# Kernel optimization log

Measured on AMD Instinct MI355X. Metric: run time of the kernel, lower is better.

The kernel has to match this reference:

```python
import jax, jax.numpy as jnp
import numpy as np

N_VARS = 2048
BATCH = 1024


def encode_input(pos):
    # pos: [n_vars, batch] -> [2*n_vars + 2, batch]
    # row 0 = 0, row 1 = 1, even rows >=2 = pos, odd rows >=3 = 1 - pos
    n = pos.shape[0]
    out = jnp.zeros((2 * n + 2,) + pos.shape[1:], dtype=pos.dtype)
    out = out.at[1].set(1.0)
    out = out.at[2::2].set(pos)
    out = out.at[3::2].set(1.0 - pos)
    return out


def setup_inputs() -> dict:
    key = jax.random.key(0)
    k0, k1, k2, k3, k4 = jax.random.split(key, 5)
    x = jax.random.uniform(k0, (N_VARS, BATCH), dtype=jnp.float32)
    idx0 = jax.random.randint(k1, (32768, 2), 0, 2 * N_VARS + 2, dtype=jnp.int32)
    idx1 = jax.random.randint(k2, (16384, 2), 0, 32768, dtype=jnp.int32)
    idx2 = jax.random.randint(k3, (8192, 2), 0, 16384, dtype=jnp.int32)
    idx3 = jax.random.randint(k4, (4096, 2), 0, 8192, dtype=jnp.int32)
    return {"x": x, "idx0": idx0, "idx1": idx1, "idx2": idx2, "idx3": idx3}


def reference(x, idx0, idx1, idx2, idx3):
    h = encode_input(x)                  # [2*n_vars+2, B]
    h = h[idx0].prod(axis=1)             # ProductLayer: [32768, B]
    h = h[idx1].sum(axis=1)              # SumLayer:     [16384, B]
    h = h[idx2].prod(axis=1)             # ProductLayer: [8192, B]
    h = h[idx3].sum(axis=1)              # SumLayer:     [4096, B]
    return h
```

## Files before the change

kernel.cpp:

```cpp
#include <hip/hip_runtime.h>
#include <hip/hip_fp16.h>

#define BATCH  1024
#define NVARS  2048
#define N_OUT  4096

typedef float f32x4 __attribute__((ext_vector_type(4)));

__device__ __forceinline__ __half2 u2h2(unsigned u) {
    union { unsigned u; __half2 h; } c; c.u = u; return c.h;
}
__device__ __forceinline__ unsigned h22u(__half2 h) {
    union { unsigned u; __half2 h; } c; c.h = h; return c.u;
}

__global__ void prep_kernel(const float* __restrict__ x,
                            const int2* __restrict__ idx0,
                            const int2* __restrict__ idx1,
                            const int2* __restrict__ idx2,
                            const int2* __restrict__ idx3,
                            unsigned* __restrict__ T,
                            unsigned* __restrict__ xh)
{
    const int gtid = blockIdx.x * blockDim.x + threadIdx.x;

    {
        const float4* x4 = (const float4*)x;
        float4 a = x4[(size_t)gtid * 2];
        float4 b = x4[(size_t)gtid * 2 + 1];
        uint4 w;
        w.x = h22u(__floats2half2_rn(a.x, a.y));
        w.y = h22u(__floats2half2_rn(a.z, a.w));
        w.z = h22u(__floats2half2_rn(b.x, b.y));
        w.w = h22u(__floats2half2_rn(b.z, b.w));
        reinterpret_cast<uint4*>(xh)[gtid] = w;
    }

    if (gtid < N_OUT) {
        const int i = gtid;
        int2 p3 = idx3[i];
        int n = 0;
        #pragma unroll
        for (int t = 0; t < 2; ++t) {
            int2 p2 = idx2[t ? p3.y : p3.x];
            #pragma unroll
            for (int u = 0; u < 2; ++u) {
                int2 p1 = idx1[u ? p2.y : p2.x];
                #pragma unroll
                for (int v = 0; v < 2; ++v) {
                    int2 p0 = idx0[v ? p1.y : p1.x];
                    unsigned w = 0;
                    #pragma unroll
                    for (int e = 0; e < 2; ++e) {
                        int k = e ? p0.y : p0.x;
                        unsigned code;
                        if (k < 2) code = (unsigned)k << 11;
                        else       code = ((2u + (k & 1)) << 11) | ((unsigned)(k - 2) >> 1);
                        w |= code << (16 * e);
                    }
                    T[(size_t)i * 8 + n] = w;
                    ++n;
                }
            }
        }
    }
}

__device__ __forceinline__ void sel2sc(unsigned sel, unsigned& s, unsigned& c) {
    c = (sel & 1u) ? 0x3C003C00u : 0u;
    s = (sel == 2u) ? 0x3C003C00u : (sel == 3u) ? 0xBC00BC00u : 0u;
}

__global__ __launch_bounds__(256) void knowledge_main(
    const char* __restrict__ xh,
    const uint4* __restrict__ T4,
    float* __restrict__ out)
{
    const int bx  = blockIdx.x;
    const int tid = threadIdx.x;
    const int octet = bx & 15;
    const int o     = (bx >> 4) * 32 + (tid >> 3);
    const int cg    = octet * 8 + (tid & 7);
    const char* base = xh + cg * 16;

    uint4 t0 = T4[(size_t)o * 2];
    uint4 t1 = T4[(size_t)o * 2 + 1];
    const unsigned tw[8] = {t0.x, t0.y, t0.z, t0.w, t1.x, t1.y, t1.z, t1.w};

    uint4 Aw[8], Bw[8];
    #pragma unroll
    for (int m = 0; m < 8; ++m) {
        unsigned w = tw[m];
        Aw[m] = *reinterpret_cast<const uint4*>(base + ((w & 0x7FFu) << 11));
        Bw[m] = *reinterpret_cast<const uint4*>(base + (((w >> 16) & 0x7FFu) << 11));
    }

    float2 accf[4];
    #pragma unroll
    for (int k = 0; k < 4; ++k) accf[k] = make_float2(0.f, 0.f);

    #pragma unroll
    for (int a3 = 0; a3 < 2; ++a3) {
        __half2 prod2[4];
        #pragma unroll
        for (int a2 = 0; a2 < 2; ++a2) {
            __half2 sum1[4];
            #pragma unroll
            for (int a1 = 0; a1 < 2; ++a1) {
                const int m = a3 * 4 + a2 * 2 + a1;
                unsigned w = tw[m];
                unsigned sa, ca, sb, cb;
                sel2sc((w >> 11) & 3u, sa, ca);
                sel2sc((w >> 27) & 3u, sb, cb);
                __half2 sA = u2h2(sa), cA = u2h2(ca);
                __half2 sB = u2h2(sb), cB = u2h2(cb);
                const unsigned aw[4] = {Aw[m].x, Aw[m].y, Aw[m].z, Aw[m].w};
                const unsigned bw[4] = {Bw[m].x, Bw[m].y, Bw[m].z, Bw[m].w};
                #pragma unroll
                for (int k = 0; k < 4; ++k) {
                    __half2 va = __hfma2(u2h2(aw[k]), sA, cA);
                    __half2 vb = __hfma2(u2h2(bw[k]), sB, cB);
                    __half2 p  = __hmul2(va, vb);
                    if (a1 == 0) sum1[k] = p;
                    else         sum1[k] = __hadd2(sum1[k], p);
                }
            }
            #pragma unroll
            for (int k = 0; k < 4; ++k) {
                if (a2 == 0) prod2[k] = sum1[k];
                else         prod2[k] = __hmul2(prod2[k], sum1[k]);
            }
        }
        #pragma unroll
        for (int k = 0; k < 4; ++k) {
            float2 pf = __half22float2(prod2[k]);
            accf[k].x += pf.x; accf[k].y += pf.y;
        }
    }

    float* dst = out + (size_t)o * BATCH + cg * 8;
    f32x4 o0 = {accf[0].x, accf[0].y, accf[1].x, accf[1].y};
    f32x4 o1 = {accf[2].x, accf[2].y, accf[3].x, accf[3].y};
    __builtin_nontemporal_store(o0, reinterpret_cast<f32x4*>(dst));
    __builtin_nontemporal_store(o1, reinterpret_cast<f32x4*>(dst) + 1);
}

__device__ __forceinline__ float Hval(int k, const float* __restrict__ x, int b) {
    if (k < 2) return (float)k;
    float v = x[((k - 2) >> 1) * BATCH + b];
    return (k & 1) ? 1.0f - v : v;
}

__global__ __launch_bounds__(256) void knowledge_fused_kernel(
    const float* __restrict__ x,
    const int2* __restrict__ idx0,
    const int2* __restrict__ idx1,
    const int2* __restrict__ idx2,
    const int2* __restrict__ idx3,
    float* __restrict__ out)
{
    const int i = blockIdx.x;
    const int b = blockIdx.y * blockDim.x + threadIdx.x;
    const int2 p3 = idx3[i];
    float acc3 = 0.0f;
    #pragma unroll
    for (int t = 0; t < 2; ++t) {
        const int2 p2 = idx2[t ? p3.y : p3.x];
        float prod2 = 1.0f;
        #pragma unroll
        for (int u = 0; u < 2; ++u) {
            const int2 p1 = idx1[u ? p2.y : p2.x];
            float sum1 = 0.0f;
            #pragma unroll
            for (int v = 0; v < 2; ++v) {
                const int2 p0 = idx0[v ? p1.y : p1.x];
                sum1 += Hval(p0.x, x, b) * Hval(p0.y, x, b);
            }
            prod2 *= sum1;
        }
        acc3 += prod2;
    }
    out[(size_t)i * BATCH + b] = acc3;
}

extern "C" void kernel_launch(void* const* d_in, const int* in_sizes, int n_in,
                              void* d_out, int out_size, void* d_ws, size_t ws_size,
                              hipStream_t stream) {
    const float* x    = (const float*)d_in[0];
    const int2*  idx0 = (const int2*)d_in[1];
    const int2*  idx1 = (const int2*)d_in[2];
    const int2*  idx2 = (const int2*)d_in[3];
    const int2*  idx3 = (const int2*)d_in[4];
    float* out = (float*)d_out;

    const size_t t_bytes  = (size_t)N_OUT * 8 * sizeof(unsigned);
    const size_t xh_bytes = (size_t)NVARS * BATCH * sizeof(__half);
    if (ws_size >= t_bytes + xh_bytes) {
        unsigned* T  = (unsigned*)d_ws;
        unsigned* xh = (unsigned*)((char*)d_ws + t_bytes);
        prep_kernel<<<(NVARS * BATCH / 8) / 256, 256, 0, stream>>>(
            x, idx0, idx1, idx2, idx3, T, xh);
        knowledge_main<<<2048, 256, 0, stream>>>(
            (const char*)xh, (const uint4*)T, out);
    } else {
        dim3 grid(N_OUT, BATCH / 256);
        knowledge_fused_kernel<<<grid, 256, 0, stream>>>(x, idx0, idx1, idx2, idx3, out);
    }
}
```

Baseline: 20.73 us.

## Stage batch-column windows of half-precision input in LDS for gather reuse

The prep kernel now writes the half-precision input in a windowed layout of 8 batch columns per window, contiguous across all variables. Each main-kernel block copies one 32 KB window into shared memory and serves 256 outputs by gathering from LDS, with 4 threads per output each handling 2 columns. This replaces scattered 16-byte global gathers per output with LDS reads. The trade-offs are a 32 KB LDS footprint per block, which limits occupancy, redundant window loads across the 16 chunk blocks, and narrower float2 output stores.

```diff
diff --git a/kernel.cpp b/kernel.cpp
--- a/kernel.cpp
+++ b/kernel.cpp
@@ -5,7 +5,11 @@
 #define NVARS  2048
 #define N_OUT  4096
 
-typedef float f32x4 __attribute__((ext_vector_type(4)));
+#define WIN_COLS 8
+#define NWIN     (BATCH / WIN_COLS)
+#define WBYTES   (NVARS * WIN_COLS * 2)
+#define CHUNK    256
+#define NCHUNK   (N_OUT / CHUNK)
 
 __device__ __forceinline__ __half2 u2h2(unsigned u) {
     union { unsigned u; __half2 h; } c; c.u = u; return c.h;
@@ -20,20 +24,22 @@
                             const int2* __restrict__ idx2,
                             const int2* __restrict__ idx3,
                             unsigned* __restrict__ T,
-                            unsigned* __restrict__ xh)
+                            char* __restrict__ xh2)
 {
     const int gtid = blockIdx.x * blockDim.x + threadIdx.x;
+    const int r  = gtid >> 7;
+    const int c8 = gtid & 127;
 
     {
         const float4* x4 = (const float4*)x;
-        float4 a = x4[(size_t)gtid * 2];
-        float4 b = x4[(size_t)gtid * 2 + 1];
+        float4 a = x4[(size_t)r * 256 + c8 * 2];
+        float4 b = x4[(size_t)r * 256 + c8 * 2 + 1];
         uint4 w;
         w.x = h22u(__floats2half2_rn(a.x, a.y));
         w.y = h22u(__floats2half2_rn(a.z, a.w));
         w.z = h22u(__floats2half2_rn(b.x, b.y));
         w.w = h22u(__floats2half2_rn(b.z, b.w));
-        reinterpret_cast<uint4*>(xh)[gtid] = w;
+        *reinterpret_cast<uint4*>(xh2 + (size_t)c8 * WBYTES + r * 16) = w;
     }
 
     if (gtid < N_OUT) {
@@ -72,77 +78,77 @@
 }
 
 __global__ __launch_bounds__(256) void knowledge_main(
-    const char* __restrict__ xh,
+    const char* __restrict__ xh2,
     const uint4* __restrict__ T4,
     float* __restrict__ out)
 {
-    const int bx  = blockIdx.x;
-    const int tid = threadIdx.x;
-    const int octet = bx & 15;
-    const int o     = (bx >> 4) * 32 + (tid >> 3);
-    const int cg    = octet * 8 + (tid & 7);
-    const char* base = xh + cg * 16;
-
-    uint4 t0 = T4[(size_t)o * 2];
-    uint4 t1 = T4[(size_t)o * 2 + 1];
-    const unsigned tw[8] = {t0.x, t0.y, t0.z, t0.w, t1.x, t1.y, t1.z, t1.w};
-
-    uint4 Aw[8], Bw[8];
+    __shared__ char xs[WBYTES];
+
+    const int bx    = blockIdx.x;
+    const int tid   = threadIdx.x;
+    const int win   = bx >> 4;
+    const int chunk = bx & 15;
+
+    {
+        const char* src = xh2 + (size_t)win * WBYTES;
+        const int w    = tid >> 6;
+        const int lane = tid & 63;
+        #pragma unroll
+        for (int p = 0; p < 8; ++p) {
+            const int off = w * 8192 + p * 1024 + lane * 16;
+            *reinterpret_cast<uint4*>(xs + off) =
+                *reinterpret_cast<const uint4*>(src + off);
+        }
+    }
+    __syncthreads();
+
+    const int cp = tid & 3;
+    const int ol = tid >> 2;
+
     #pragma unroll
-    for (int m = 0; m < 8; ++m) {
-        unsigned w = tw[m];
-        Aw[m] = *reinterpret_cast<const uint4*>(base + ((w & 0x7FFu) << 11));
-        Bw[m] = *reinterpret_cast<const uint4*>(base + (((w >> 16) & 0x7FFu) << 11));
-    }
-
-    float2 accf[4];
-    #pragma unroll
-    for (int k = 0; k < 4; ++k) accf[k] = make_float2(0.f, 0.f);
-
-    #pragma unroll
-    for (int a3 = 0; a3 < 2; ++a3) {
-        __half2 prod2[4];
-        #pragma unroll
-        for (int a2 = 0; a2 < 2; ++a2) {
-            __half2 sum1[4];
+    for (int pass = 0; pass < 4; ++pass) {
+        const int o = chunk * CHUNK + pass * 64 + ol;
+        uint4 t0 = T4[(size_t)o * 2];
+        uint4 t1 = T4[(size_t)o * 2 + 1];
+        const unsigned tw[8] = {t0.x, t0.y, t0.z, t0.w, t1.x, t1.y, t1.z, t1.w};
+
+        __half2 av[8], bv[8];
+        #pragma unroll
+        for (int m = 0; m < 8; ++m) {
+            unsigned w = tw[m];
+            av[m] = *reinterpret_cast<const __half2*>(
+                        xs + ((w & 0x7FFu) << 4) + cp * 4);
+            bv[m] = *reinterpret_cast<const __half2*>(
+                        xs + (((w >> 16) & 0x7FFu) << 4) + cp * 4);
+        }
+
+        float2 accf = make_float2(0.f, 0.f);
+        #pragma unroll
+        for (int a3 = 0; a3 < 2; ++a3) {
+            __half2 prod2;
             #pragma unroll
-            for (int a1 = 0; a1 < 2; ++a1) {
-                const int m = a3 * 4 + a2 * 2 + a1;
-                unsigned w = tw[m];
-                unsigned sa, ca, sb, cb;
-                sel2sc((w >> 11) & 3u, sa, ca);
-                sel2sc((w >> 27) & 3u, sb, cb);
-                __half2 sA = u2h2(sa), cA = u2h2(ca);
-                __half2 sB = u2h2(sb), cB = u2h2(cb);
-                const unsigned aw[4] = {Aw[m].x, Aw[m].y, Aw[m].z, Aw[m].w};
-                const unsigned bw[4] = {Bw[m].x, Bw[m].y, Bw[m].z, Bw[m].w};
+            for (int a2 = 0; a2 < 2; ++a2) {
+                __half2 sum1;
                 #pragma unroll
-                for (int k = 0; k < 4; ++k) {
-                    __half2 va = __hfma2(u2h2(aw[k]), sA, cA);
-                    __half2 vb = __hfma2(u2h2(bw[k]), sB, cB);
+                for (int a1 = 0; a1 < 2; ++a1) {
+                    const int m = a3 * 4 + a2 * 2 + a1;
+                    unsigned w = tw[m];
+                    unsigned sa, ca, sb, cb;
+                    sel2sc((w >> 11) & 3u, sa, ca);
+                    sel2sc((w >> 27) & 3u, sb, cb);
+                    __half2 va = __hfma2(av[m], u2h2(sa), u2h2(ca));
+                    __half2 vb = __hfma2(bv[m], u2h2(sb), u2h2(cb));
                     __half2 p  = __hmul2(va, vb);
-                    if (a1 == 0) sum1[k] = p;
-                    else         sum1[k] = __hadd2(sum1[k], p);
+                    sum1 = (a1 == 0) ? p : __hadd2(sum1, p);
                 }
+                prod2 = (a2 == 0) ? sum1 : __hmul2(prod2, sum1);
             }
-            #pragma unroll
-            for (int k = 0; k < 4; ++k) {
-                if (a2 == 0) prod2[k] = sum1[k];
-                else         prod2[k] = __hmul2(prod2[k], sum1[k]);
-            }
-        }
-        #pragma unroll
-        for (int k = 0; k < 4; ++k) {
-            float2 pf = __half22float2(prod2[k]);
-            accf[k].x += pf.x; accf[k].y += pf.y;
-        }
-    }
-
-    float* dst = out + (size_t)o * BATCH + cg * 8;
-    f32x4 o0 = {accf[0].x, accf[0].y, accf[1].x, accf[1].y};
-    f32x4 o1 = {accf[2].x, accf[2].y, accf[3].x, accf[3].y};
-    __builtin_nontemporal_store(o0, reinterpret_cast<f32x4*>(dst));
-    __builtin_nontemporal_store(o1, reinterpret_cast<f32x4*>(dst) + 1);
+            float2 pf = __half22float2(prod2);
+            accf.x += pf.x; accf.y += pf.y;
+        }
+
+        *reinterpret_cast<float2*>(out + (size_t)o * BATCH + win * 8 + cp * 2) = accf;
+    }
 }
 
 __device__ __forceinline__ float Hval(int k, const float* __restrict__ x, int b) {
@@ -193,15 +199,15 @@
     const int2*  idx3 = (const int2*)d_in[4];
     float* out = (float*)d_out;
 
-    const size_t t_bytes  = (size_t)N_OUT * 8 * sizeof(unsigned);
-    const size_t xh_bytes = (size_t)NVARS * BATCH * sizeof(__half);
-    if (ws_size >= t_bytes + xh_bytes) {
-        unsigned* T  = (unsigned*)d_ws;
-        unsigned* xh = (unsigned*)((char*)d_ws + t_bytes);
+    const size_t t_bytes   = (size_t)N_OUT * 8 * sizeof(unsigned);
+    const size_t xh2_bytes = (size_t)NWIN * WBYTES;
+    if (ws_size >= t_bytes + xh2_bytes) {
+        unsigned* T   = (unsigned*)d_ws;
+        char*     xh2 = (char*)d_ws + t_bytes;
         prep_kernel<<<(NVARS * BATCH / 8) / 256, 256, 0, stream>>>(
-            x, idx0, idx1, idx2, idx3, T, xh);
-        knowledge_main<<<2048, 256, 0, stream>>>(
-            (const char*)xh, (const uint4*)T, out);
+            x, idx0, idx1, idx2, idx3, T, xh2);
+        knowledge_main<<<NWIN * NCHUNK, 256, 0, stream>>>(
+            xh2, (const uint4*)T, out);
     } else {
         dim3 grid(N_OUT, BATCH / 256);
         knowledge_fused_kernel<<<grid, 256, 0, stream>>>(x, idx0, idx1, idx2, idx3, out);
```

New measurement: 32.83 us. +58.4%, slower.

## Transpose fp16 input into batch-chunk-major layout and remap work per thread

Applied to the files above, without the earlier changes.

The prep kernel now converts x to fp16 and transposes it through shared memory into a layout where each 8-sample batch chunk of all variables is contiguous (32 KB slabs). The main kernel assigns one output node per thread and loops over four batch chunks. Each slab is prefetched cooperatively so gathers hit L1/L2, and results are staged through shared memory so stores are coalesced. The aim is better locality for the random gathers, at the cost of a shared-memory transpose, higher register pressure (32 accumulators) and far fewer blocks (256), which lowers occupancy.

```diff
diff --git a/kernel.cpp b/kernel.cpp
--- a/kernel.cpp
+++ b/kernel.cpp
@@ -5,6 +5,9 @@
 #define NVARS  2048
 #define N_OUT  4096
 
+#define W8BYTES (NVARS * 16)
+#define NW8     (BATCH / 8)
+
 typedef float f32x4 __attribute__((ext_vector_type(4)));
 
 __device__ __forceinline__ __half2 u2h2(unsigned u) {
@@ -13,31 +16,30 @@
 __device__ __forceinline__ unsigned h22u(__half2 h) {
     union { unsigned u; __half2 h; } c; c.h = h; return c.u;
 }
-
-__global__ void prep_kernel(const float* __restrict__ x,
-                            const int2* __restrict__ idx0,
-                            const int2* __restrict__ idx1,
-                            const int2* __restrict__ idx2,
-                            const int2* __restrict__ idx3,
-                            unsigned* __restrict__ T,
-                            unsigned* __restrict__ xh)
+__device__ __forceinline__ void sel2sc(unsigned sel, unsigned& s, unsigned& c) {
+    c = (sel & 1u) ? 0x3C003C00u : 0u;
+    s = (sel == 2u) ? 0x3C003C00u : (sel == 3u) ? 0xBC00BC00u : 0u;
+}
+
+__global__ __launch_bounds__(256) void prep_kernel(
+    const float* __restrict__ x,
+    const int2* __restrict__ idx0,
+    const int2* __restrict__ idx1,
+    const int2* __restrict__ idx2,
+    const int2* __restrict__ idx3,
+    unsigned* __restrict__ T,
+    char* __restrict__ xh2)
 {
-    const int gtid = blockIdx.x * blockDim.x + threadIdx.x;
-
-    {
-        const float4* x4 = (const float4*)x;
-        float4 a = x4[(size_t)gtid * 2];
-        float4 b = x4[(size_t)gtid * 2 + 1];
-        uint4 w;
-        w.x = h22u(__floats2half2_rn(a.x, a.y));
-        w.y = h22u(__floats2half2_rn(a.z, a.w));
-        w.z = h22u(__floats2half2_rn(b.x, b.y));
-        w.w = h22u(__floats2half2_rn(b.z, b.w));
-        reinterpret_cast<uint4*>(xh)[gtid] = w;
-    }
-
-    if (gtid < N_OUT) {
-        const int i = gtid;
+    __shared__ char tile[64 * 272];
+
+    const int bid = blockIdx.x;
+    const int tid = threadIdx.x;
+    const int rt  = bid >> 3;
+    const int ct  = bid & 7;
+    const int r0  = rt * 64;
+
+    if (bid < 16) {
+        const int i = bid * 256 + tid;
         int2 p3 = idx3[i];
         int n = 0;
         #pragma unroll
@@ -64,85 +66,145 @@
             }
         }
     }
-}
-
-__device__ __forceinline__ void sel2sc(unsigned sel, unsigned& s, unsigned& c) {
-    c = (sel & 1u) ? 0x3C003C00u : 0u;
-    s = (sel == 2u) ? 0x3C003C00u : (sel == 3u) ? 0xBC00BC00u : 0u;
-}
-
-__global__ __launch_bounds__(256) void knowledge_main(
-    const char* __restrict__ xh,
+
+    {
+        const int r_l = tid >> 5;
+        const int c4  = tid & 31;
+        #pragma unroll
+        for (int q = 0; q < 8; ++q) {
+            const int rr = q * 8 + r_l;
+            float4 v = ((const float4*)x)[(size_t)(r0 + rr) * 256 + ct * 32 + c4];
+            unsigned h0 = h22u(__floats2half2_rn(v.x, v.y));
+            unsigned h1 = h22u(__floats2half2_rn(v.z, v.w));
+            unsigned* p = (unsigned*)(tile + rr * 272 + c4 * 8);
+            p[0] = h0; p[1] = h1;
+        }
+    }
+    __syncthreads();
+
+    {
+        const int r2 = tid & 63;
+        const int wl = tid >> 6;
+        #pragma unroll
+        for (int pp = 0; pp < 4; ++pp) {
+            const int w08l = pp * 4 + wl;
+            uint4 v = *(const uint4*)(tile + r2 * 272 + w08l * 16);
+            const int w08 = ct * 16 + w08l;
+            *(uint4*)(xh2 + (size_t)w08 * W8BYTES + (r0 + r2) * 16) = v;
+        }
+    }
+}
+
+__global__ __launch_bounds__(512) void knowledge_main(
+    const char* __restrict__ xh2,
     const uint4* __restrict__ T4,
     float* __restrict__ out)
 {
-    const int bx  = blockIdx.x;
+    __shared__ char st[4][64 * 144];
+
+    const int b   = blockIdx.x;
     const int tid = threadIdx.x;
-    const int octet = bx & 15;
-    const int o     = (bx >> 4) * 32 + (tid >> 3);
-    const int cg    = octet * 8 + (tid & 7);
-    const char* base = xh + cg * 16;
+    const int cb  = b & 31;
+    const int oc  = b >> 5;
+    const int o   = oc * 512 + tid;
 
     uint4 t0 = T4[(size_t)o * 2];
     uint4 t1 = T4[(size_t)o * 2 + 1];
     const unsigned tw[8] = {t0.x, t0.y, t0.z, t0.w, t1.x, t1.y, t1.z, t1.w};
 
-    uint4 Aw[8], Bw[8];
+    int offA[8], offB[8];
+    unsigned sA[8], cA[8], sB[8], cB[8];
     #pragma unroll
     for (int m = 0; m < 8; ++m) {
-        unsigned w = tw[m];
-        Aw[m] = *reinterpret_cast<const uint4*>(base + ((w & 0x7FFu) << 11));
-        Bw[m] = *reinterpret_cast<const uint4*>(base + (((w >> 16) & 0x7FFu) << 11));
-    }
-
-    float2 accf[4];
+        offA[m] = (int)((tw[m] & 0x7FFu) << 4);
+        offB[m] = (int)(((tw[m] >> 16) & 0x7FFu) << 4);
+        sel2sc((tw[m] >> 11) & 3u, sA[m], cA[m]);
+        sel2sc((tw[m] >> 27) & 3u, sB[m], cB[m]);
+    }
+
+    float acc[32];
+
     #pragma unroll
-    for (int k = 0; k < 4; ++k) accf[k] = make_float2(0.f, 0.f);
-
-    #pragma unroll
-    for (int a3 = 0; a3 < 2; ++a3) {
-        __half2 prod2[4];
-        #pragma unroll
-        for (int a2 = 0; a2 < 2; ++a2) {
-            __half2 sum1[4];
-            #pragma unroll
-            for (int a1 = 0; a1 < 2; ++a1) {
-                const int m = a3 * 4 + a2 * 2 + a1;
-                unsigned w = tw[m];
-                unsigned sa, ca, sb, cb;
-                sel2sc((w >> 11) & 3u, sa, ca);
-                sel2sc((w >> 27) & 3u, sb, cb);
-                __half2 sA = u2h2(sa), cA = u2h2(ca);
-                __half2 sB = u2h2(sb), cB = u2h2(cb);
-                const unsigned aw[4] = {Aw[m].x, Aw[m].y, Aw[m].z, Aw[m].w};
-                const unsigned bw[4] = {Bw[m].x, Bw[m].y, Bw[m].z, Bw[m].w};
+    for (int p = 0; p < 4; ++p) {
+        const char* base = xh2 + (size_t)(cb * 4 + p) * W8BYTES;
+
+        {
+            const uint4* src = (const uint4*)base + tid * 4;
+            uint4 pa = src[0], pb = src[1], pc = src[2], pd = src[3];
+            asm volatile("" :: "v"(pa.x), "v"(pa.y), "v"(pa.z), "v"(pa.w),
+                               "v"(pb.x), "v"(pb.y), "v"(pb.z), "v"(pb.w),
+                               "v"(pc.x), "v"(pc.y), "v"(pc.z), "v"(pc.w),
+                               "v"(pd.x), "v"(pd.y), "v"(pd.z), "v"(pd.w));
+        }
+
+        uint4 Av[8], Bv[8];
+        #pragma unroll
+        for (int m = 0; m < 8; ++m) {
+            Av[m] = *(const uint4*)(base + offA[m]);
+            Bv[m] = *(const uint4*)(base + offB[m]);
+        }
+
+        float accp[8];
+        #pragma unroll
+        for (int k2 = 0; k2 < 8; ++k2) accp[k2] = 0.f;
+
+        #pragma unroll
+        for (int a3 = 0; a3 < 2; ++a3) {
+            __half2 prod2[4];
+            #pragma unroll
+            for (int a2 = 0; a2 < 2; ++a2) {
+                __half2 sum1[4];
                 #pragma unroll
-                for (int k = 0; k < 4; ++k) {
-                    __half2 va = __hfma2(u2h2(aw[k]), sA, cA);
-                    __half2 vb = __hfma2(u2h2(bw[k]), sB, cB);
-                    __half2 p  = __hmul2(va, vb);
-                    if (a1 == 0) sum1[k] = p;
-                    else         sum1[k] = __hadd2(sum1[k], p);
+                for (int a1 = 0; a1 < 2; ++a1) {
+                    const int m = a3 * 4 + a2 * 2 + a1;
+                    const unsigned aw[4] = {Av[m].x, Av[m].y, Av[m].z, Av[m].w};
+                    const unsigned bw[4] = {Bv[m].x, Bv[m].y, Bv[m].z, Bv[m].w};
+                    #pragma unroll
+                    for (int k = 0; k < 4; ++k) {
+                        __half2 va = __hfma2(u2h2(aw[k]), u2h2(sA[m]), u2h2(cA[m]));
+                        __half2 vb = __hfma2(u2h2(bw[k]), u2h2(sB[m]), u2h2(cB[m]));
+                        __half2 pr = __hmul2(va, vb);
+                        sum1[k] = (a1 == 0) ? pr : __hadd2(sum1[k], pr);
+                    }
                 }
+                #pragma unroll
+                for (int k = 0; k < 4; ++k)
+                    prod2[k] = (a2 == 0) ? sum1[k] : __hmul2(prod2[k], sum1[k]);
             }
             #pragma unroll
             for (int k = 0; k < 4; ++k) {
-                if (a2 == 0) prod2[k] = sum1[k];
-                else         prod2[k] = __hmul2(prod2[k], sum1[k]);
-            }
-        }
-        #pragma unroll
-        for (int k = 0; k < 4; ++k) {
-            float2 pf = __half22float2(prod2[k]);
-            accf[k].x += pf.x; accf[k].y += pf.y;
-        }
-    }
-
-    float* dst = out + (size_t)o * BATCH + cg * 8;
-    f32x4 o0 = {accf[0].x, accf[0].y, accf[1].x, accf[1].y};
-    f32x4 o1 = {accf[2].x, accf[2].y, accf[3].x, accf[3].y};
-    __builtin_nontemporal_store(o0, reinterpret_cast<f32x4*>(dst));
-    __builtin_nontemporal_store(o1, reinterpret_cast<f32x4*>(dst) + 1);
+                float2 pf = __half22float2(prod2[k]);
+                accp[k * 2]     += pf.x;
+                accp[k * 2 + 1] += pf.y;
+            }
+        }
+        #pragma unroll
+        for (int k2 = 0; k2 < 8; ++k2) acc[p * 8 + k2] = accp[k2];
+    }
+
+    const int w    = tid >> 6;
+    const int lane = tid & 63;
+    char* buf = st[w & 3];
+    const size_t orow0 = (size_t)(oc * 512 + w * 64);
+
+    auto dump = [&]() {
+        #pragma unroll
+        for (int k = 0; k < 8; ++k) {
+            f32x4 v = {acc[k * 4], acc[k * 4 + 1], acc[k * 4 + 2], acc[k * 4 + 3]};
+            *reinterpret_cast<f32x4*>(buf + lane * 144 + k * 16) = v;
+        }
+        #pragma unroll
+        for (int j = 0; j < 8; ++j) {
+            const int r     = j * 8 + (lane >> 3);
+            const int piece = lane & 7;
+            f32x4 v = *reinterpret_cast<const f32x4*>(buf + r * 144 + piece * 16);
+            float* dst = out + (orow0 + r) * BATCH + cb * 32 + piece * 4;
+            __builtin_nontemporal_store(v, reinterpret_cast<f32x4*>(dst));
+        }
+    };
+    if (w < 4) dump();
+    __syncthreads();
+    if (w >= 4) dump();
 }
 
 __device__ __forceinline__ float Hval(int k, const float* __restrict__ x, int b) {
@@ -193,15 +255,13 @@
     const int2*  idx3 = (const int2*)d_in[4];
     float* out = (float*)d_out;
 
-    const size_t t_bytes  = (size_t)N_OUT * 8 * sizeof(unsigned);
-    const size_t xh_bytes = (size_t)NVARS * BATCH * sizeof(__half);
-    if (ws_size >= t_bytes + xh_bytes) {
-        unsigned* T  = (unsigned*)d_ws;
-        unsigned* xh = (unsigned*)((char*)d_ws + t_bytes);
-        prep_kernel<<<(NVARS * BATCH / 8) / 256, 256, 0, stream>>>(
-            x, idx0, idx1, idx2, idx3, T, xh);
-        knowledge_main<<<2048, 256, 0, stream>>>(
-            (const char*)xh, (const uint4*)T, out);
+    const size_t t_bytes   = (size_t)N_OUT * 8 * sizeof(unsigned);
+    const size_t xh2_bytes = (size_t)NW8 * W8BYTES;
+    if (ws_size >= t_bytes + xh2_bytes) {
+        unsigned* T   = (unsigned*)d_ws;
+        char*     xh2 = (char*)d_ws + t_bytes;
+        prep_kernel<<<256, 256, 0, stream>>>(x, idx0, idx1, idx2, idx3, T, xh2);
+        knowledge_main<<<256, 512, 0, stream>>>(xh2, (const uint4*)T, out);
     } else {
         dim3 grid(N_OUT, BATCH / 256);
         knowledge_fused_kernel<<<grid, 256, 0, stream>>>(x, idx0, idx1, idx2, idx3, out);
```

New measurement: 28.18 us. 36.0% more time.
